# Kernel optimization log

Hardware: AMD Instinct MI355X
Metric: run time of the kernel (lower is better)

The kernel has to match this reference:

```python
import jax, jax.numpy as jnp
import numpy as np

D_MODEL = 1024
NUM_HEADS = 16
D_K = D_MODEL // NUM_HEADS
BATCH = 2
SEQ = 2048


def setup_inputs() -> dict:
    key = jax.random.key(0)
    ks = jax.random.split(key, 9)
    s = 1.0 / np.sqrt(D_MODEL)
    X = jax.random.normal(ks[0], (BATCH, SEQ, D_MODEL), dtype=jnp.float32)
    # causal mask, broadcastable over batch and heads; 0 means masked
    mask = jnp.tril(jnp.ones((SEQ, SEQ), dtype=jnp.int32))[None, None]
    W_Q = jax.random.uniform(ks[1], (D_MODEL, D_MODEL), jnp.float32, -s, s)
    b_Q = jax.random.uniform(ks[2], (D_MODEL,), jnp.float32, -s, s)
    W_K = jax.random.uniform(ks[3], (D_MODEL, D_MODEL), jnp.float32, -s, s)
    b_K = jax.random.uniform(ks[4], (D_MODEL,), jnp.float32, -s, s)
    W_V = jax.random.uniform(ks[5], (D_MODEL, D_MODEL), jnp.float32, -s, s)
    b_V = jax.random.uniform(ks[6], (D_MODEL,), jnp.float32, -s, s)
    W_O = jax.random.uniform(ks[7], (D_MODEL, D_MODEL), jnp.float32, -s, s)
    b_O = jax.random.uniform(ks[8], (D_MODEL,), jnp.float32, -s, s)
    return {"X": X, "mask": mask, "W_Q": W_Q, "b_Q": b_Q, "W_K": W_K,
            "b_K": b_K, "W_V": W_V, "b_V": b_V, "W_O": W_O, "b_O": b_O}


def reference(X, mask, W_Q, b_Q, W_K, b_K, W_V, b_V, W_O, b_O):
    B, S, _ = X.shape
    H, Dk = NUM_HEADS, D_K
    # projections; torch Linear uses y = x @ W.T + b; here W_* is stored as [in, out]
    Q = (X @ W_Q + b_Q).reshape(B, S, H, Dk).transpose(0, 2, 1, 3)  # [B,H,S,Dk]
    K = (X @ W_K + b_K).reshape(B, S, H, Dk).transpose(0, 2, 1, 3)
    V = (X @ W_V + b_V).reshape(B, S, H, Dk).transpose(0, 2, 1, 3)
    scores = jnp.einsum("bhqd,bhkd->bhqk", Q, K) / jnp.sqrt(jnp.asarray(Dk, X.dtype))
    scores = jnp.where(mask == 0, -jnp.inf, scores)
    attn = jax.nn.softmax(scores, axis=-1)  # [B,H,S,S]
    out = jnp.einsum("bhqk,bhkd->bhqd", attn, V)
    out = out.transpose(0, 2, 1, 3).reshape(B, S, H * Dk)
    return out @ W_O + b_O
```

## Files before the change

kernel.cpp:

```cpp
#include <hip/hip_runtime.h>
#include <math.h>

#define S_LEN 2048
#define DM 1024
#define NH 16
#define DK 64
#define BB 2
#define MROWS (BB * S_LEN)
#define QTILES (S_LEN / 64)
#define LOG2E 1.44269504088896340736f

typedef __attribute__((ext_vector_type(8))) short bf16x8;
typedef __attribute__((ext_vector_type(4))) float f32x4;

__device__ __forceinline__ unsigned short f2bf(float f) {
    unsigned int u = __builtin_bit_cast(unsigned int, f);
    u += 0x7fff + ((u >> 16) & 1);
    return (unsigned short)(u >> 16);
}

__device__ __forceinline__ float hw_exp2(float x) {
    return __builtin_amdgcn_exp2f(x);
}

__device__ __forceinline__ void gload_lds16(const unsigned short* g, unsigned short* l) {
    __builtin_amdgcn_global_load_lds(
        (const __attribute__((address_space(1))) unsigned int*)(const void*)g,
        (__attribute__((address_space(3))) unsigned int*)(void*)l, 16, 0, 0);
}

__global__ __launch_bounds__(256) void prep_kernel(
    const float* __restrict__ X, unsigned short* __restrict__ Xb,
    const float* __restrict__ W_Q, const float* __restrict__ W_K,
    const float* __restrict__ W_V, const float* __restrict__ W_O,
    unsigned short* __restrict__ WqkvT, unsigned short* __restrict__ WoT) {
    const int z = blockIdx.z;
    if (z == 0) {
        int i = (blockIdx.x * 256 + threadIdx.x) * 4;
        float4 v = *(const float4*)(X + i);
        ushort4 o;
        o.x = f2bf(v.x); o.y = f2bf(v.y); o.z = f2bf(v.z); o.w = f2bf(v.w);
        *(ushort4*)(Xb + i) = o;
        return;
    }
    if (blockIdx.x >= (DM / 64) * (DM / 64)) return;
    const float* in = z == 1 ? W_Q : (z == 2 ? W_K : (z == 3 ? W_V : W_O));
    unsigned short* out = z == 4 ? WoT : (WqkvT + (size_t)(z - 1) * DM * DM);
    __shared__ float tile[64][65];
    const int bx = blockIdx.x & 15, by = blockIdx.x >> 4;
    const int tx = threadIdx.x & 63, ty = threadIdx.x >> 6;
#pragma unroll
    for (int i = 0; i < 64; i += 4)
        tile[ty + i][tx] = in[(size_t)(by * 64 + ty + i) * DM + bx * 64 + tx];
    __syncthreads();
#pragma unroll
    for (int i = 0; i < 64; i += 4)
        out[(size_t)(bx * 64 + ty + i) * DM + by * 64 + tx] = f2bf(tile[tx][ty + i]);
}

__global__ __launch_bounds__(256) void gemm_qkv_kernel(
    const unsigned short* __restrict__ A,
    const unsigned short* __restrict__ Bt,
    const float* __restrict__ bQ, const float* __restrict__ bK,
    const float* __restrict__ bV,
    unsigned short* __restrict__ outQ, unsigned short* __restrict__ outK,
    unsigned short* __restrict__ outV) {
    const int K = DM;
    __shared__ __align__(16) unsigned short smem[4 * 64 * 72];
    const int tid = threadIdx.x;
    const int wave = tid >> 6, lane = tid & 63;
    const int lq = lane >> 4, ln = lane & 15;
    const int m0 = blockIdx.y * 128, n0 = blockIdx.x * 128;
    const int wr = (wave >> 1) * 64, wc = (wave & 1) * 64;

    f32x4 acc[4][4];
#pragma unroll
    for (int i = 0; i < 4; ++i)
#pragma unroll
        for (int j = 0; j < 4; ++j)
            acc[i][j] = (f32x4){0.f, 0.f, 0.f, 0.f};

    const unsigned short* ga = A  + (size_t)(m0 + (tid >> 2)) * K + (tid & 3) * 8;
    const unsigned short* gb = Bt + (size_t)(n0 + (tid >> 2)) * K + (tid & 3) * 8;
    const size_t half = (size_t)64 * K;

    {
        unsigned short* An = smem;
        unsigned short* Bn = smem + 4096;
        gload_lds16(ga, An + tid * 8);
        gload_lds16(ga + half, An + 2048 + tid * 8);
        gload_lds16(gb, Bn + tid * 8);
        gload_lds16(gb + half, Bn + 2048 + tid * 8);
    }

    for (int k0 = 0; k0 < K; k0 += 32) {
        const int cur = (k0 >> 5) & 1;
        unsigned short* As = smem + cur * 8192;
        unsigned short* Bs = As + 4096;
        __syncthreads();
        if (k0 + 32 < K) {
            unsigned short* An = smem + (cur ^ 1) * 8192;
            unsigned short* Bn = An + 4096;
            gload_lds16(ga + k0 + 32, An + tid * 8);
            gload_lds16(ga + half + k0 + 32, An + 2048 + tid * 8);
            gload_lds16(gb + k0 + 32, Bn + tid * 8);
            gload_lds16(gb + half + k0 + 32, Bn + 2048 + tid * 8);
        }
        bf16x8 af[4], bfv[4];
#pragma unroll
        for (int i = 0; i < 4; ++i) af[i]  = *(const bf16x8*)&As[(wr + i * 16 + ln) * 32 + lq * 8];
#pragma unroll
        for (int j = 0; j < 4; ++j) bfv[j] = *(const bf16x8*)&Bs[(wc + j * 16 + ln) * 32 + lq * 8];
#pragma unroll
        for (int i = 0; i < 4; ++i)
#pragma unroll
            for (int j = 0; j < 4; ++j)
                acc[i][j] = __builtin_amdgcn_mfma_f32_16x16x32_bf16(af[i], bfv[j], acc[i][j], 0, 0, 0);
    }
    __syncthreads();

    const int which = n0 >> 10;
    const float* bias = which == 0 ? bQ : (which == 1 ? bK : bV);
    const float scale = which == 0 ? 0.125f * LOG2E : 1.0f;
    unsigned short* ob = which == 0 ? outQ : (which == 1 ? outK : outV);
    unsigned short* Ts = &smem[wave * 64 * 72];
#pragma unroll
    for (int i = 0; i < 4; ++i)
#pragma unroll
        for (int j = 0; j < 4; ++j)
#pragma unroll
            for (int r = 0; r < 4; ++r) {
                int rl = i * 16 + lq * 4 + r;
                int cl = j * 16 + ln;
                float v = (acc[i][j][r] + bias[(n0 & 1023) + wc + cl]) * scale;
                if (which == 2) Ts[cl * 72 + rl] = f2bf(v);
                else            Ts[rl * 72 + cl] = f2bf(v);
            }
    const int hh = ((n0 & 1023) + wc) >> 6;
    const int bI = (m0 + wr) >> 11, sbase = (m0 + wr) & 2047;
    if (which <= 1) {
        unsigned short* dst = ob + ((size_t)(bI * NH + hh) * S_LEN + sbase) * DK;
#pragma unroll
        for (int t = 0; t < 8; ++t) {
            int rl = t * 8 + (lane >> 3);
            *(uint4*)(dst + rl * DK + (lane & 7) * 8) =
                *(const uint4*)&Ts[rl * 72 + (lane & 7) * 8];
        }
    } else {
        unsigned short* dst = ob + ((size_t)(bI * NH + hh) * DK) * S_LEN + sbase;
#pragma unroll
        for (int t = 0; t < 8; ++t) {
            int dkl = t * 8 + (lane >> 3);
            *(uint4*)(dst + (size_t)dkl * S_LEN + (lane & 7) * 8) =
                *(const uint4*)&Ts[dkl * 72 + (lane & 7) * 8];
        }
    }
}

__global__ __launch_bounds__(256) void gemm_o_kernel(
    const unsigned short* __restrict__ A,
    const unsigned short* __restrict__ Bt,
    const float* __restrict__ bias,
    float* __restrict__ out_f) {
    const int K = DM;
    __shared__ __align__(16) unsigned short smem[2 * 6144];
    const int tid = threadIdx.x;
    const int wave = tid >> 6, lane = tid & 63;
    const int lq = lane >> 4, ln = lane & 15;
    const int m0 = blockIdx.y * 128, n0 = blockIdx.x * 64;
    const int wr = (wave >> 1) * 64, wc = (wave & 1) * 32;

    f32x4 acc[4][2];
#pragma unroll
    for (int i = 0; i < 4; ++i)
#pragma unroll
        for (int j = 0; j < 2; ++j)
            acc[i][j] = (f32x4){0.f, 0.f, 0.f, 0.f};

    const unsigned short* ga = A  + (size_t)(m0 + (tid >> 2)) * K + (tid & 3) * 8;
    const unsigned short* gb = Bt + (size_t)(n0 + (tid >> 2)) * K + (tid & 3) * 8;
    const size_t half = (size_t)64 * K;

    {
        unsigned short* An = smem;
        gload_lds16(ga, An + tid * 8);
        gload_lds16(ga + half, An + 2048 + tid * 8);
        gload_lds16(gb, An + 4096 + tid * 8);
    }

    for (int k0 = 0; k0 < K; k0 += 32) {
        const int cur = (k0 >> 5) & 1;
        unsigned short* As = smem + cur * 6144;
        unsigned short* Bs = As + 4096;
        __syncthreads();
        if (k0 + 32 < K) {
            unsigned short* An = smem + (cur ^ 1) * 6144;
            gload_lds16(ga + k0 + 32, An + tid * 8);
            gload_lds16(ga + half + k0 + 32, An + 2048 + tid * 8);
            gload_lds16(gb + k0 + 32, An + 4096 + tid * 8);
        }
        bf16x8 af[4], bfv[2];
#pragma unroll
        for (int i = 0; i < 4; ++i) af[i]  = *(const bf16x8*)&As[(wr + i * 16 + ln) * 32 + lq * 8];
#pragma unroll
        for (int j = 0; j < 2; ++j) bfv[j] = *(const bf16x8*)&Bs[(wc + j * 16 + ln) * 32 + lq * 8];
#pragma unroll
        for (int i = 0; i < 4; ++i)
#pragma unroll
            for (int j = 0; j < 2; ++j)
                acc[i][j] = __builtin_amdgcn_mfma_f32_16x16x32_bf16(af[i], bfv[j], acc[i][j], 0, 0, 0);
    }

#pragma unroll
    for (int i = 0; i < 4; ++i)
#pragma unroll
        for (int j = 0; j < 2; ++j)
#pragma unroll
            for (int r = 0; r < 4; ++r) {
                int m = m0 + wr + i * 16 + lq * 4 + r;
                int n = n0 + wc + j * 16 + ln;
                out_f[(size_t)m * DM + n] = acc[i][j][r] + bias[n];
            }
}

__global__ __launch_bounds__(512, 4) void attn_kernel(
    const unsigned short* __restrict__ Qg,
    const unsigned short* __restrict__ Kg,
    const unsigned short* __restrict__ Vg,
    unsigned short* __restrict__ Og) {
    __shared__ __align__(16) unsigned short KBUF[2 * 128 * 64];
    __shared__ __align__(16) unsigned short VBUF[2 * 64 * 128];
    __shared__ __align__(16) unsigned short Pw[8 * 640];

    const int tid = threadIdx.x;
    const int wave = tid >> 6, lane = tid & 63;
    const int lq = lane >> 4, ln = lane & 15;
    const int bh = blockIdx.x, b = bh >> 4, h = bh & 15;
    const int j = blockIdx.y;
    const int grp = wave >> 2, wv = wave & 3;
    const int qt = grp == 0 ? (QTILES - 1 - j) : j;
    const int nkv_me = grp == 0 ? ((33 - j) >> 1) : ((j + 2) >> 1);
    const int T = (33 - j) >> 1;

    const unsigned short* Qb = Qg + (size_t)bh * S_LEN * DK;
    const unsigned short* Kb = Kg + (size_t)bh * S_LEN * DK;
    const unsigned short* Vb = Vg + (size_t)bh * DK * S_LEN;

    const int krow_l = lane >> 3;
    const int kchunk = (lane & 7) ^ krow_l;
    const int vrow_l = lane >> 4;

    {
#pragma unroll
        for (int s = 0; s < 2; ++s)
            gload_lds16(Kb + (size_t)(wave * 16 + s * 8 + krow_l) * DK + kchunk * 8,
                        KBUF + (wave * 16 + s * 8) * 64 + lane * 8);
#pragma unroll
        for (int s = 0; s < 2; ++s) {
            int rv = wave * 8 + s * 4 + vrow_l;
            int c  = (lane & 15) ^ (rv & 15);
            gload_lds16(Vb + (size_t)rv * S_LEN + c * 8,
                        VBUF + (wave * 8 + s * 4) * 128 + lane * 8);
        }
    }

    const int q0 = qt * 64;
    bf16x8 qf0 = *(const bf16x8*)(Qb + (q0 + wv * 16 + ln) * DK + lq * 8);
    bf16x8 qf1 = *(const bf16x8*)(Qb + (q0 + wv * 16 + ln) * DK + 32 + lq * 8);

    const short one_bf = (short)0x3F80;
    const bf16x8 onesf = {one_bf, one_bf, one_bf, one_bf,
                          one_bf, one_bf, one_bf, one_bf};

    f32x4 oacc[4];
    f32x4 lacc = (f32x4){0.f, 0.f, 0.f, 0.f};
#pragma unroll
    for (int i = 0; i < 4; ++i) oacc[i] = (f32x4){0.f, 0.f, 0.f, 0.f};

    for (int g = 0; g < T; ++g) {
        const int cur = g & 1;
        unsigned short* Kl = KBUF + cur * 8192;
        unsigned short* Vl = VBUF + cur * 8192;
        __syncthreads();

        if (g + 1 < T) {
            const int kv0n = (g + 1) * 128;
            unsigned short* Kn = KBUF + (cur ^ 1) * 8192;
            unsigned short* Vn = VBUF + (cur ^ 1) * 8192;
#pragma unroll
            for (int s = 0; s < 2; ++s)
                gload_lds16(Kb + (size_t)(kv0n + wave * 16 + s * 8 + krow_l) * DK + kchunk * 8,
                            Kn + (wave * 16 + s * 8) * 64 + lane * 8);
#pragma unroll
            for (int s = 0; s < 2; ++s) {
                int rv = wave * 8 + s * 4 + vrow_l;
                int c  = (lane & 15) ^ (rv & 15);
                gload_lds16(Vb + (size_t)rv * S_LEN + kv0n + c * 8,
                            Vn + (wave * 8 + s * 4) * 128 + lane * 8);
            }
        }

        if (g < nkv_me) {
            const int kv0 = g * 128;

            f32x4 sc[8];
#pragma unroll
            for (int ct = 0; ct < 8; ++ct) {
                const int rbase = (ct * 16 + ln) * 64;
                bf16x8 k0 = *(const bf16x8*)&Kl[rbase + ((lq ^ (ln & 7)) * 8)];
                bf16x8 k1 = *(const bf16x8*)&Kl[rbase + (((lq + 4) ^ (ln & 7)) * 8)];
                f32x4 a = (f32x4){0.f, 0.f, 0.f, 0.f};
                a = __builtin_amdgcn_mfma_f32_16x16x32_bf16(qf0, k0, a, 0, 0, 0);
                a = __builtin_amdgcn_mfma_f32_16x16x32_bf16(qf1, k1, a, 0, 0, 0);
                sc[ct] = a;
            }

            if (g == nkv_me - 1) {
#pragma unroll
                for (int ct = 0; ct < 8; ++ct) {
                    int col = kv0 + ct * 16 + ln;
#pragma unroll
                    for (int r = 0; r < 4; ++r) {
                        int row = q0 + wv * 16 + lq * 4 + r;
                        if (col > row) sc[ct][r] = -INFINITY;
                    }
                }
            }

#pragma unroll
            for (int ct = 0; ct < 8; ++ct)
#pragma unroll
                for (int r = 0; r < 4; ++r)
                    sc[ct][r] = hw_exp2(sc[ct][r]);

            unsigned short* Pq = Pw + wave * 640;
#pragma unroll
            for (int qd = 0; qd < 4; ++qd) {
#pragma unroll
                for (int c2 = 0; c2 < 2; ++c2)
#pragma unroll
                    for (int r = 0; r < 4; ++r)
                        Pq[(lq * 4 + r) * 40 + c2 * 16 + ln] = f2bf(sc[qd * 2 + c2][r]);
                bf16x8 pf = *(const bf16x8*)&Pq[ln * 40 + lq * 8];
                lacc = __builtin_amdgcn_mfma_f32_16x16x32_bf16(pf, onesf, lacc, 0, 0, 0);
#pragma unroll
                for (int dkt = 0; dkt < 4; ++dkt) {
                    const unsigned short* vr =
                        &Vl[(dkt * 16 + ln) * 128 + (((qd * 4 + lq) ^ ln) * 8)];
                    oacc[dkt] = __builtin_amdgcn_mfma_f32_16x16x32_bf16(pf, *(const bf16x8*)vr, oacc[dkt], 0, 0, 0);
                }
            }
        }
    }

#pragma unroll
    for (int r = 0; r < 4; ++r) {
        float inv = 1.0f / lacc[r];
        int s = q0 + wv * 16 + lq * 4 + r;
#pragma unroll
        for (int dkt = 0; dkt < 4; ++dkt)
            Og[((size_t)(b * S_LEN + s)) * DM + h * 64 + dkt * 16 + ln] =
                f2bf(oacc[dkt][r] * inv);
    }
}

extern "C" void kernel_launch(void* const* d_in, const int* in_sizes, int n_in,
                              void* d_out, int out_size, void* d_ws, size_t ws_size,
                              hipStream_t stream) {
    const float* X   = (const float*)d_in[0];
    const float* W_Q = (const float*)d_in[2];
    const float* b_Q = (const float*)d_in[3];
    const float* W_K = (const float*)d_in[4];
    const float* b_K = (const float*)d_in[5];
    const float* W_V = (const float*)d_in[6];
    const float* b_V = (const float*)d_in[7];
    const float* W_O = (const float*)d_in[8];
    const float* b_O = (const float*)d_in[9];

    unsigned short* Xb    = (unsigned short*)d_ws;
    unsigned short* WqkvT = Xb    + (size_t)MROWS * DM;
    unsigned short* WoT   = WqkvT + (size_t)3 * DM * DM;
    unsigned short* Qb    = WoT   + (size_t)DM * DM;
    unsigned short* Kb    = Qb    + (size_t)MROWS * DM;
    unsigned short* Vtb   = Kb    + (size_t)MROWS * DM;
    unsigned short* Ob    = Vtb   + (size_t)MROWS * DM;

    prep_kernel<<<dim3((MROWS * DM) / 1024, 1, 5), 256, 0, stream>>>(
        X, Xb, W_Q, W_K, W_V, W_O, WqkvT, WoT);

    gemm_qkv_kernel<<<dim3(3 * DM / 128, MROWS / 128), 256, 0, stream>>>(
        Xb, WqkvT, b_Q, b_K, b_V, Qb, Kb, Vtb);

    attn_kernel<<<dim3(BB * NH, QTILES / 2), 512, 0, stream>>>(Qb, Kb, Vtb, Ob);

    gemm_o_kernel<<<dim3(DM / 64, MROWS / 128), 256, 0, stream>>>(
        Ob, WoT, b_O, (float*)d_out);
}
```

Before: 188.7 us.

## Rewrite QKV GEMM as 256x256 tile with swizzled LDS and phased prefetch pipeline

The QKV projection GEMM moves from 128x128 tiles with 4 waves and a simple double buffer to 256x256 tiles with 8 waves. The K tile grows to 64, the LDS layout is XOR-swizzled, and each K step is split into four quadrant phases that interleave async global-to-LDS prefetch with MFMA work, using explicit vmcnt waits, barriers and setprio. The aim is more data reuse per tile, fewer LDS bank conflicts and better overlap of memory with compute. The cost is heavy register pressure (128 accumulator floats per lane) and only 192 blocks, which may underfill the 256 CUs.

```diff
diff --git a/kernel.cpp b/kernel.cpp
--- a/kernel.cpp
+++ b/kernel.cpp
@@ -58,101 +58,148 @@
         out[(size_t)(bx * 64 + ty + i) * DM + by * 64 + tx] = f2bf(tile[tx][ty + i]);
 }
 
-__global__ __launch_bounds__(256) void gemm_qkv_kernel(
+#define VMCNT(N) asm volatile("s_waitcnt vmcnt(" #N ")" ::: "memory")
+
+#define QPHASE(MH_, NH_, PRESTAGE, PREWAIT) do {                               \
+    bf16x8 af_[4][2], bf_[2][2];                                               \
+    _Pragma("unroll") for (int ii = 0; ii < 4; ++ii)                           \
+    _Pragma("unroll") for (int kk = 0; kk < 2; ++kk)                           \
+        af_[ii][kk] = *(const bf16x8*)&As[(MH_) * 8192 +                       \
+            (ii * 16 + ln + wm * 64) * 64 + (((kk * 4 + lq) ^ (ln & 7)) * 8)]; \
+    _Pragma("unroll") for (int jj = 0; jj < 2; ++jj)                           \
+    _Pragma("unroll") for (int kk = 0; kk < 2; ++kk)                           \
+        bf_[jj][kk] = *(const bf16x8*)&Bs[(NH_) * 8192 +                       \
+            (jj * 16 + ln + wn * 32) * 64 + (((kk * 4 + lq) ^ (ln & 7)) * 8)]; \
+    PRESTAGE;                                                                  \
+    __builtin_amdgcn_s_barrier();                                              \
+    asm volatile("s_waitcnt lgkmcnt(0)" ::: "memory");                         \
+    __builtin_amdgcn_sched_barrier(0);                                         \
+    __builtin_amdgcn_s_setprio(1);                                             \
+    _Pragma("unroll") for (int kk = 0; kk < 2; ++kk)                           \
+    _Pragma("unroll") for (int ii = 0; ii < 4; ++ii)                           \
+    _Pragma("unroll") for (int jj = 0; jj < 2; ++jj)                           \
+        acc[(MH_) * 4 + ii][(NH_) * 2 + jj] =                                  \
+            __builtin_amdgcn_mfma_f32_16x16x32_bf16(                           \
+                af_[ii][kk], bf_[jj][kk],                                      \
+                acc[(MH_) * 4 + ii][(NH_) * 2 + jj], 0, 0, 0);                 \
+    __builtin_amdgcn_s_setprio(0);                                             \
+    PREWAIT;                                                                   \
+    __builtin_amdgcn_s_barrier();                                              \
+} while (0)
+
+__global__ __launch_bounds__(512, 2) void gemm_qkv_kernel(
     const unsigned short* __restrict__ A,
     const unsigned short* __restrict__ Bt,
     const float* __restrict__ bQ, const float* __restrict__ bK,
     const float* __restrict__ bV,
     unsigned short* __restrict__ outQ, unsigned short* __restrict__ outK,
     unsigned short* __restrict__ outV) {
-    const int K = DM;
-    __shared__ __align__(16) unsigned short smem[4 * 64 * 72];
+    __shared__ __align__(16) unsigned short smem[65536];
     const int tid = threadIdx.x;
     const int wave = tid >> 6, lane = tid & 63;
     const int lq = lane >> 4, ln = lane & 15;
-    const int m0 = blockIdx.y * 128, n0 = blockIdx.x * 128;
-    const int wr = (wave >> 1) * 64, wc = (wave & 1) * 64;
-
-    f32x4 acc[4][4];
-#pragma unroll
-    for (int i = 0; i < 4; ++i)
-#pragma unroll
-        for (int j = 0; j < 4; ++j)
-            acc[i][j] = (f32x4){0.f, 0.f, 0.f, 0.f};
-
-    const unsigned short* ga = A  + (size_t)(m0 + (tid >> 2)) * K + (tid & 3) * 8;
-    const unsigned short* gb = Bt + (size_t)(n0 + (tid >> 2)) * K + (tid & 3) * 8;
-    const size_t half = (size_t)64 * K;
-
+    const int wm = wave >> 2, wn = wave & 3;
+    const int m0 = blockIdx.y * 256, n0 = blockIdx.x * 256;
+
+    f32x4 acc[8][4];
+#pragma unroll
+    for (int i = 0; i < 8; ++i)
+#pragma unroll
+        for (int j = 0; j < 4; ++j) acc[i][j] = (f32x4){0.f, 0.f, 0.f, 0.f};
+
+    auto stageA = [&](int t, int h) {
+#pragma unroll
+        for (int s = 0; s < 2; ++s) {
+            int p = (s << 9) + tid;
+            int rp = p >> 3;
+            int grow = (rp & 63) + ((rp >> 6) << 7) + (h << 6);
+            gload_lds16(A + (size_t)(m0 + grow) * DM + (t << 6) +
+                            (((tid & 7) ^ (rp & 7)) << 3),
+                        smem + ((t & 1) << 14) + (h << 13) + (p << 3));
+        }
+    };
+    auto stageB = [&](int t, int h) {
+#pragma unroll
+        for (int s = 0; s < 2; ++s) {
+            int p = (s << 9) + tid;
+            int rp = p >> 3;
+            int grow = (rp & 31) + ((rp >> 5) << 6) + (h << 5);
+            gload_lds16(Bt + (size_t)(n0 + grow) * DM + (t << 6) +
+                            (((tid & 7) ^ (rp & 7)) << 3),
+                        smem + 32768 + ((t & 1) << 14) + (h << 13) + (p << 3));
+        }
+    };
+
+    stageB(0, 0); stageA(0, 0); stageA(0, 1); stageB(0, 1);
+    stageB(1, 0); stageA(1, 0);
+    VMCNT(4);
+    __builtin_amdgcn_s_barrier();
+
+    for (int t = 0; t < 14; ++t) {
+        const unsigned short* As = smem + ((t & 1) << 14);
+        const unsigned short* Bs = smem + 32768 + ((t & 1) << 14);
+        QPHASE(0, 0, stageA(t + 1, 1), (void)0);
+        QPHASE(1, 0, stageB(t + 1, 1), VMCNT(6));
+        QPHASE(0, 1, stageB(t + 2, 0), (void)0);
+        QPHASE(1, 1, stageA(t + 2, 0), VMCNT(6));
+    }
     {
-        unsigned short* An = smem;
-        unsigned short* Bn = smem + 4096;
-        gload_lds16(ga, An + tid * 8);
-        gload_lds16(ga + half, An + 2048 + tid * 8);
-        gload_lds16(gb, Bn + tid * 8);
-        gload_lds16(gb + half, Bn + 2048 + tid * 8);
-    }
-
-    for (int k0 = 0; k0 < K; k0 += 32) {
-        const int cur = (k0 >> 5) & 1;
-        unsigned short* As = smem + cur * 8192;
-        unsigned short* Bs = As + 4096;
-        __syncthreads();
-        if (k0 + 32 < K) {
-            unsigned short* An = smem + (cur ^ 1) * 8192;
-            unsigned short* Bn = An + 4096;
-            gload_lds16(ga + k0 + 32, An + tid * 8);
-            gload_lds16(ga + half + k0 + 32, An + 2048 + tid * 8);
-            gload_lds16(gb + k0 + 32, Bn + tid * 8);
-            gload_lds16(gb + half + k0 + 32, Bn + 2048 + tid * 8);
-        }
-        bf16x8 af[4], bfv[4];
-#pragma unroll
-        for (int i = 0; i < 4; ++i) af[i]  = *(const bf16x8*)&As[(wr + i * 16 + ln) * 32 + lq * 8];
-#pragma unroll
-        for (int j = 0; j < 4; ++j) bfv[j] = *(const bf16x8*)&Bs[(wc + j * 16 + ln) * 32 + lq * 8];
-#pragma unroll
-        for (int i = 0; i < 4; ++i)
-#pragma unroll
-            for (int j = 0; j < 4; ++j)
-                acc[i][j] = __builtin_amdgcn_mfma_f32_16x16x32_bf16(af[i], bfv[j], acc[i][j], 0, 0, 0);
-    }
-    __syncthreads();
+        const unsigned short* As = smem;
+        const unsigned short* Bs = smem + 32768;
+        QPHASE(0, 0, stageA(15, 1), (void)0);
+        QPHASE(1, 0, stageB(15, 1), VMCNT(6));
+        QPHASE(0, 1, (void)0, (void)0);
+        QPHASE(1, 1, (void)0, VMCNT(2));
+    }
+    {
+        const unsigned short* As = smem + 16384;
+        const unsigned short* Bs = smem + 32768 + 16384;
+        QPHASE(0, 0, (void)0, (void)0);
+        QPHASE(1, 0, (void)0, VMCNT(0));
+        QPHASE(0, 1, (void)0, (void)0);
+        QPHASE(1, 1, (void)0, (void)0);
+    }
 
     const int which = n0 >> 10;
     const float* bias = which == 0 ? bQ : (which == 1 ? bK : bV);
     const float scale = which == 0 ? 0.125f * LOG2E : 1.0f;
     unsigned short* ob = which == 0 ? outQ : (which == 1 ? outK : outV);
-    unsigned short* Ts = &smem[wave * 64 * 72];
-#pragma unroll
-    for (int i = 0; i < 4; ++i)
-#pragma unroll
-        for (int j = 0; j < 4; ++j)
-#pragma unroll
-            for (int r = 0; r < 4; ++r) {
-                int rl = i * 16 + lq * 4 + r;
-                int cl = j * 16 + ln;
-                float v = (acc[i][j][r] + bias[(n0 & 1023) + wc + cl]) * scale;
-                if (which == 2) Ts[cl * 72 + rl] = f2bf(v);
-                else            Ts[rl * 72 + cl] = f2bf(v);
-            }
-    const int hh = ((n0 & 1023) + wc) >> 6;
-    const int bI = (m0 + wr) >> 11, sbase = (m0 + wr) & 2047;
-    if (which <= 1) {
-        unsigned short* dst = ob + ((size_t)(bI * NH + hh) * S_LEN + sbase) * DK;
-#pragma unroll
-        for (int t = 0; t < 8; ++t) {
-            int rl = t * 8 + (lane >> 3);
-            *(uint4*)(dst + rl * DK + (lane & 7) * 8) =
-                *(const uint4*)&Ts[rl * 72 + (lane & 7) * 8];
-        }
-    } else {
-        unsigned short* dst = ob + ((size_t)(bI * NH + hh) * DK) * S_LEN + sbase;
-#pragma unroll
-        for (int t = 0; t < 8; ++t) {
-            int dkl = t * 8 + (lane >> 3);
-            *(uint4*)(dst + (size_t)dkl * S_LEN + (lane & 7) * 8) =
-                *(const uint4*)&Ts[dkl * 72 + (lane & 7) * 8];
+    unsigned short* Ts = smem + wave * 4608;
+    const int nb = (n0 & 1023) + wn * 64;
+    const int hh = nb >> 6;
+    const int bI = (m0 + wm * 128) >> 11;
+    const int sb = (m0 + wm * 128) & 2047;
+#pragma unroll
+    for (int ih = 0; ih < 2; ++ih) {
+#pragma unroll
+        for (int i2 = 0; i2 < 4; ++i2)
+#pragma unroll
+            for (int j = 0; j < 4; ++j)
+#pragma unroll
+                for (int r = 0; r < 4; ++r) {
+                    int rl = i2 * 16 + lq * 4 + r;
+                    int cl = j * 16 + ln;
+                    float v = (acc[ih * 4 + i2][j][r] + bias[nb + cl]) * scale;
+                    if (which == 2) Ts[cl * 72 + rl] = f2bf(v);
+                    else            Ts[rl * 72 + cl] = f2bf(v);
+                }
+        const int sfull = sb + ih * 64;
+        if (which <= 1) {
+            unsigned short* dst = ob + ((size_t)(bI * NH + hh) * S_LEN + sfull) * DK;
+#pragma unroll
+            for (int t8 = 0; t8 < 8; ++t8) {
+                int rl = t8 * 8 + (lane >> 3);
+                *(uint4*)(dst + rl * DK + (lane & 7) * 8) =
+                    *(const uint4*)&Ts[rl * 72 + (lane & 7) * 8];
+            }
+        } else {
+            unsigned short* dst = ob + ((size_t)(bI * NH + hh) * DK) * S_LEN + sfull;
+#pragma unroll
+            for (int t8 = 0; t8 < 8; ++t8) {
+                int dkl = t8 * 8 + (lane >> 3);
+                *(uint4*)(dst + (size_t)dkl * S_LEN + (lane & 7) * 8) =
+                    *(const uint4*)&Ts[dkl * 72 + (lane & 7) * 8];
+            }
         }
     }
 }
@@ -388,7 +435,7 @@
     prep_kernel<<<dim3((MROWS * DM) / 1024, 1, 5), 256, 0, stream>>>(
         X, Xb, W_Q, W_K, W_V, W_O, WqkvT, WoT);
 
-    gemm_qkv_kernel<<<dim3(3 * DM / 128, MROWS / 128), 256, 0, stream>>>(
+    gemm_qkv_kernel<<<dim3(3 * DM / 256, MROWS / 256), 512, 0, stream>>>(
         Xb, WqkvT, b_Q, b_K, b_V, Qb, Kb, Vtb);
 
     attn_kernel<<<dim3(BB * NH, QTILES / 2), 512, 0, stream>>>(Qb, Kb, Vtb, Ob);
```

After: 191.5 us. About the same (+1.4%).
